# Optimization experiments

Hardware: AMD Instinct MI355X
Metric: run time of the kernel (lower is better)

Reference implementation:

```python
import jax, jax.numpy as jnp
import numpy as np

B, H, S, D = 2, 16, 1024, 64  # batch, n_heads, seq_len, d_k
NEG = -1.0e9


def setup_inputs() -> dict:
    key = jax.random.key(0)
    kq, kk, kv, kt, kf, km, kd = jax.random.split(key, 7)
    Q = jax.random.normal(kq, (B, H, S, D), dtype=jnp.float32)
    K = jax.random.normal(kk, (B, H, S, D), dtype=jnp.float32)
    V = jax.random.normal(kv, (B, H, S, D), dtype=jnp.float32)
    ia_type = jax.random.normal(kt, (B, H, S, S), dtype=jnp.float32)
    ia_feat = jax.random.normal(kf, (B, H, S, S), dtype=jnp.float32)
    attn_mask_if = jax.random.bernoulli(km, 0.1, (B, H, S, S))
    attn_mask = attn_mask_if  # passed to forward but unused, as in the source
    distance_matrix = jax.random.normal(kd, (B, S, S), dtype=jnp.float32)
    return {"Q": Q, "K": K, "V": V, "attn_mask": attn_mask,
            "attn_mask_if": attn_mask_if, "ia_type": ia_type,
            "ia_feat": ia_feat, "distance_matrix": distance_matrix}


def reference(Q, K, V, attn_mask, attn_mask_if, ia_type, ia_feat, distance_matrix):
    # scores1 = Q K^T / sqrt(d_k)
    scores1 = jnp.einsum("bhqd,bhkd->bhqk", Q, K) / jnp.sqrt(jnp.float32(D))
    # bias masked to -1e9, then scores masked again to -1e9 => masked entries are exactly -1e9
    scores = jnp.where(attn_mask_if, NEG, scores1 + ia_type + ia_feat)
    attn = jax.nn.softmax(scores, axis=-1)
    context = jnp.einsum("bhqk,bhkd->bhqd", attn, V)
    return context, attn
```

## Files before the change

### kernel.cpp

```cpp
#include <hip/hip_runtime.h>
#include <math.h>

#define S_LEN 1024
#define D_DIM 64
#define NEGV  (-1.0e9f)

__global__ __launch_bounds__(256, 2)
void attn_bias_fused(const float* __restrict__ Q, const float* __restrict__ K,
                     const float* __restrict__ V, const int* __restrict__ mif,
                     const float* __restrict__ iat, const float* __restrict__ iaf,
                     float* __restrict__ ctx, float* __restrict__ attn)
{
    __shared__ float4 Kt4[D_DIM][64];
    __shared__ float  SB[2048];

    float* Pn = (float*)Kt4;
    float (*Qst)[16] = (float(*)[16])SB;

    const int tid  = threadIdx.x;
    const int wave = tid >> 6;
    const int lane = tid & 63;
    const int bh   = blockIdx.x >> 6;
    const int qb   = (blockIdx.x & 63) << 4;

    const float* Qb = Q + ((size_t)(bh * S_LEN + qb)) * D_DIM;
    const float* Kb = K + ((size_t)bh * S_LEN) * D_DIM;
    const float* Vb = V + ((size_t)bh * S_LEN) * D_DIM;

    {
        int q = tid >> 4, l = tid & 15;
        float4 v = *(const float4*)(Qb + (size_t)q * D_DIM + l * 4);
        Qst[4 * l + 0][q] = v.x;
        Qst[4 * l + 1][q] = v.y;
        Qst[4 * l + 2][q] = v.z;
        Qst[4 * l + 3][q] = v.w;
    }

    const int kg = lane;
    const int qg = wave;

    float4 sc[16];

    #pragma unroll
    for (int c = 0; c < 4; ++c) {
        __syncthreads();
        {
            int l = tid & 15, kr0 = tid >> 4;
            #pragma unroll
            for (int i = 0; i < 16; ++i) {
                int kk = i * 16 + kr0;
                float4 v = *(const float4*)(Kb + (size_t)(c * 256 + kk) * D_DIM + l * 4);
                int cc  = (kk >> 2) ^ (l & 7);
                int sub = kk & 3;
                ((float*)&Kt4[4 * l + 0][cc])[sub] = v.x;
                ((float*)&Kt4[4 * l + 1][cc])[sub] = v.y;
                ((float*)&Kt4[4 * l + 2][cc])[sub] = v.z;
                ((float*)&Kt4[4 * l + 3][cc])[sub] = v.w;
            }
        }
        __syncthreads();

        float4 bt[4], bf[4];
        int4   bm[4];
        #pragma unroll
        for (int i = 0; i < 4; ++i) {
            size_t off = ((size_t)(bh * S_LEN + qb + qg * 4 + i)) * S_LEN + c * 256 + kg * 4;
            bt[i] = *(const float4*)(iat + off);
            bf[i] = *(const float4*)(iaf + off);
            bm[i] = *(const int4*)(mif + off);
        }

        float4 a0 = {0.f, 0.f, 0.f, 0.f}, a1 = a0, a2 = a0, a3 = a0;
        #pragma unroll 16
        for (int d = 0; d < D_DIM; ++d) {
            float4 kv = Kt4[d][kg ^ ((d >> 2) & 7)];
            float4 qv = *(const float4*)&Qst[d][qg * 4];
            a0.x = fmaf(qv.x, kv.x, a0.x); a0.y = fmaf(qv.x, kv.y, a0.y);
            a0.z = fmaf(qv.x, kv.z, a0.z); a0.w = fmaf(qv.x, kv.w, a0.w);
            a1.x = fmaf(qv.y, kv.x, a1.x); a1.y = fmaf(qv.y, kv.y, a1.y);
            a1.z = fmaf(qv.y, kv.z, a1.z); a1.w = fmaf(qv.y, kv.w, a1.w);
            a2.x = fmaf(qv.z, kv.x, a2.x); a2.y = fmaf(qv.z, kv.y, a2.y);
            a2.z = fmaf(qv.z, kv.z, a2.z); a2.w = fmaf(qv.z, kv.w, a2.w);
            a3.x = fmaf(qv.w, kv.x, a3.x); a3.y = fmaf(qv.w, kv.y, a3.y);
            a3.z = fmaf(qv.w, kv.z, a3.z); a3.w = fmaf(qv.w, kv.w, a3.w);
        }

        float4 av[4] = {a0, a1, a2, a3};
        #pragma unroll
        for (int i = 0; i < 4; ++i) {
            float4 s = av[i];
            float4 t = bt[i], f = bf[i];
            int4   m = bm[i];
            s.x = m.x ? NEGV : fmaf(s.x, 0.125f, t.x + f.x);
            s.y = m.y ? NEGV : fmaf(s.y, 0.125f, t.y + f.y);
            s.z = m.z ? NEGV : fmaf(s.z, 0.125f, t.z + f.z);
            s.w = m.w ? NEGV : fmaf(s.w, 0.125f, t.w + f.w);
            sc[c * 4 + i] = s;
        }
    }
    __syncthreads();

    {
        float mx[4], sum[4], rinv[4];
        #pragma unroll
        for (int i = 0; i < 4; ++i) {
            float m = -INFINITY;
            #pragma unroll
            for (int c = 0; c < 4; ++c) {
                float4 v = sc[c * 4 + i];
                m = fmaxf(m, fmaxf(fmaxf(v.x, v.y), fmaxf(v.z, v.w)));
            }
            #pragma unroll
            for (int s = 1; s < 64; s <<= 1) m = fmaxf(m, __shfl_xor(m, s, 64));
            mx[i] = m;
        }
        #pragma unroll
        for (int i = 0; i < 4; ++i) {
            float sm = 0.f;
            #pragma unroll
            for (int c = 0; c < 4; ++c) {
                float4 v = sc[c * 4 + i];
                v.x = __expf(v.x - mx[i]);
                v.y = __expf(v.y - mx[i]);
                v.z = __expf(v.z - mx[i]);
                v.w = __expf(v.w - mx[i]);
                sc[c * 4 + i] = v;
                sm += v.x + v.y + v.z + v.w;
            }
            #pragma unroll
            for (int s = 1; s < 64; s <<= 1) sm += __shfl_xor(sm, s, 64);
            sum[i] = sm;
            rinv[i] = 1.f / sm;
        }
        #pragma unroll
        for (int i = 0; i < 4; ++i) {
            int r = qg * 4 + i;
            float* arow = attn + ((size_t)(bh * S_LEN + qb + r)) * S_LEN;
            #pragma unroll
            for (int c = 0; c < 4; ++c) {
                float4 v = sc[c * 4 + i];
                v.x *= rinv[i]; v.y *= rinv[i]; v.z *= rinv[i]; v.w *= rinv[i];
                *(float4*)(arow + c * 256 + kg * 4)  = v;
                *(float4*)&Pn[r * 1024 + c * 256 + kg * 4] = v;
            }
        }
        (void)sum;
    }
    __syncthreads();

    {
        int dg = lane & 15;
        int ks = lane >> 4;
        float4 acc[16];
        #pragma unroll
        for (int q = 0; q < 16; ++q) acc[q] = make_float4(0.f, 0.f, 0.f, 0.f);

        #pragma unroll 2
        for (int i = 0; i < 16; ++i) {
            int k0 = wave * 256 + i * 16 + ks * 4;
            const float* vrow = Vb + (size_t)k0 * D_DIM + dg * 4;
            float4 v0 = *(const float4*)(vrow + 0 * D_DIM);
            float4 v1 = *(const float4*)(vrow + 1 * D_DIM);
            float4 v2 = *(const float4*)(vrow + 2 * D_DIM);
            float4 v3 = *(const float4*)(vrow + 3 * D_DIM);
            #pragma unroll
            for (int q = 0; q < 16; ++q) {
                float4 p = *(const float4*)&Pn[q * 1024 + k0];
                float4 a = acc[q];
                a.x = fmaf(p.x, v0.x, a.x); a.x = fmaf(p.y, v1.x, a.x);
                a.x = fmaf(p.z, v2.x, a.x); a.x = fmaf(p.w, v3.x, a.x);
                a.y = fmaf(p.x, v0.y, a.y); a.y = fmaf(p.y, v1.y, a.y);
                a.y = fmaf(p.z, v2.y, a.y); a.y = fmaf(p.w, v3.y, a.y);
                a.z = fmaf(p.x, v0.z, a.z); a.z = fmaf(p.y, v1.z, a.z);
                a.z = fmaf(p.z, v2.z, a.z); a.z = fmaf(p.w, v3.z, a.z);
                a.w = fmaf(p.x, v0.w, a.w); a.w = fmaf(p.y, v1.w, a.w);
                a.w = fmaf(p.z, v2.w, a.w); a.w = fmaf(p.w, v3.w, a.w);
                acc[q] = a;
            }
        }

        #pragma unroll
        for (int q = 0; q < 16; ++q) {
            acc[q].x += __shfl_xor(acc[q].x, 16, 64);
            acc[q].y += __shfl_xor(acc[q].y, 16, 64);
            acc[q].z += __shfl_xor(acc[q].z, 16, 64);
            acc[q].w += __shfl_xor(acc[q].w, 16, 64);
            acc[q].x += __shfl_xor(acc[q].x, 32, 64);
            acc[q].y += __shfl_xor(acc[q].y, 32, 64);
            acc[q].z += __shfl_xor(acc[q].z, 32, 64);
            acc[q].w += __shfl_xor(acc[q].w, 32, 64);
        }

        float* scratch = SB;
        #pragma unroll
        for (int qh = 0; qh < 2; ++qh) {
            __syncthreads();
            if (lane < 16) {
                #pragma unroll
                for (int j = 0; j < 8; ++j)
                    *(float4*)&scratch[(wave * 8 + j) * 64 + dg * 4] = acc[qh * 8 + j];
            }
            __syncthreads();
            if (tid < 128) {
                int qq = tid >> 4;
                int dr = tid & 15;
                float4 r = make_float4(0.f, 0.f, 0.f, 0.f);
                #pragma unroll
                for (int s = 0; s < 4; ++s) {
                    float4 v = *(const float4*)&scratch[(s * 8 + qq) * 64 + dr * 4];
                    r.x += v.x; r.y += v.y; r.z += v.z; r.w += v.w;
                }
                *(float4*)(ctx + ((size_t)(bh * S_LEN + qb + qh * 8 + qq)) * D_DIM + dr * 4) = r;
            }
        }
    }
}

extern "C" void kernel_launch(void* const* d_in, const int* in_sizes, int n_in,
                              void* d_out, int out_size, void* d_ws, size_t ws_size,
                              hipStream_t stream) {
    const float* Q   = (const float*)d_in[0];
    const float* K   = (const float*)d_in[1];
    const float* V   = (const float*)d_in[2];
    const int*   mif = (const int*)d_in[4];
    const float* iat = (const float*)d_in[5];
    const float* iaf = (const float*)d_in[6];

    float* ctx  = (float*)d_out;
    float* attn = (float*)d_out + (size_t)2 * 16 * 1024 * 64;

    dim3 grid(2048), block(256);
    hipLaunchKernelGGL(attn_bias_fused, grid, block, 0, stream,
                       Q, K, V, mif, iat, iaf, ctx, attn);
}
```

Baseline: 536.8 us.

## Use 512-thread blocks of 32 query rows and read P back from global

Each block now has 512 threads and covers 32 query rows instead of 16, so every K tile staged in shared memory serves twice as many rows. The normalized probabilities are no longer copied into LDS; the P·V stage reads them back from the attn output just written to global memory. The context reduction is restructured so all waves write partial sums to a larger scratch area before one final reduction, which removes several barriers. Risks: the much tighter launch bound (512, 4) likely caps VGPRs low enough to cause spills with 16 float4 score registers, and P now costs extra L2 traffic.

```diff
diff --git a/kernel.cpp b/kernel.cpp
--- a/kernel.cpp
+++ b/kernel.cpp
@@ -5,7 +5,7 @@
 #define D_DIM 64
 #define NEGV  (-1.0e9f)
 
-__global__ __launch_bounds__(256, 2)
+__global__ __launch_bounds__(512, 4)
 void attn_bias_fused(const float* __restrict__ Q, const float* __restrict__ K,
                      const float* __restrict__ V, const int* __restrict__ mif,
                      const float* __restrict__ iat, const float* __restrict__ iaf,
@@ -14,14 +14,14 @@
     __shared__ float4 Kt4[D_DIM][64];
     __shared__ float  SB[2048];
 
-    float* Pn = (float*)Kt4;
-    float (*Qst)[16] = (float(*)[16])SB;
+    float (*Qst)[32] = (float(*)[32])SB;
+    float* scr = (float*)Kt4;
 
     const int tid  = threadIdx.x;
     const int wave = tid >> 6;
     const int lane = tid & 63;
-    const int bh   = blockIdx.x >> 6;
-    const int qb   = (blockIdx.x & 63) << 4;
+    const int bh   = blockIdx.x >> 5;
+    const int qb   = (blockIdx.x & 31) << 5;
 
     const float* Qb = Q + ((size_t)(bh * S_LEN + qb)) * D_DIM;
     const float* Kb = K + ((size_t)bh * S_LEN) * D_DIM;
@@ -47,8 +47,8 @@
         {
             int l = tid & 15, kr0 = tid >> 4;
             #pragma unroll
-            for (int i = 0; i < 16; ++i) {
-                int kk = i * 16 + kr0;
+            for (int i = 0; i < 8; ++i) {
+                int kk = i * 32 + kr0;
                 float4 v = *(const float4*)(Kb + (size_t)(c * 256 + kk) * D_DIM + l * 4);
                 int cc  = (kk >> 2) ^ (l & 7);
                 int sub = kk & 3;
@@ -98,7 +98,6 @@
             sc[c * 4 + i] = s;
         }
     }
-    __syncthreads();
 
     {
         float mx[4], sum[4], rinv[4];
@@ -140,8 +139,7 @@
             for (int c = 0; c < 4; ++c) {
                 float4 v = sc[c * 4 + i];
                 v.x *= rinv[i]; v.y *= rinv[i]; v.z *= rinv[i]; v.w *= rinv[i];
-                *(float4*)(arow + c * 256 + kg * 4)  = v;
-                *(float4*)&Pn[r * 1024 + c * 256 + kg * 4] = v;
+                *(float4*)(arow + c * 256 + kg * 4) = v;
             }
         }
         (void)sum;
@@ -149,70 +147,71 @@
     __syncthreads();
 
     {
-        int dg = lane & 15;
-        int ks = lane >> 4;
-        float4 acc[16];
-        #pragma unroll
-        for (int q = 0; q < 16; ++q) acc[q] = make_float4(0.f, 0.f, 0.f, 0.f);
-
-        #pragma unroll 2
-        for (int i = 0; i < 16; ++i) {
-            int k0 = wave * 256 + i * 16 + ks * 4;
-            const float* vrow = Vb + (size_t)k0 * D_DIM + dg * 4;
-            float4 v0 = *(const float4*)(vrow + 0 * D_DIM);
-            float4 v1 = *(const float4*)(vrow + 1 * D_DIM);
-            float4 v2 = *(const float4*)(vrow + 2 * D_DIM);
-            float4 v3 = *(const float4*)(vrow + 3 * D_DIM);
+        const int dg = lane & 15;
+        const int ks = lane >> 4;
+        for (int h = 0; h < 2; ++h) {
+            float4 acc[16];
+            #pragma unroll
+            for (int q = 0; q < 16; ++q) acc[q] = make_float4(0.f, 0.f, 0.f, 0.f);
+
+            const float* pb = attn + ((size_t)(bh * S_LEN + qb + h * 16)) * S_LEN;
+
+            #pragma unroll 2
+            for (int i = 0; i < 8; ++i) {
+                int k0 = wave * 128 + i * 16 + ks * 4;
+                const float* vrow = Vb + (size_t)k0 * D_DIM + dg * 4;
+                float4 v0 = *(const float4*)(vrow + 0 * D_DIM);
+                float4 v1 = *(const float4*)(vrow + 1 * D_DIM);
+                float4 v2 = *(const float4*)(vrow + 2 * D_DIM);
+                float4 v3 = *(const float4*)(vrow + 3 * D_DIM);
+                #pragma unroll
+                for (int q = 0; q < 16; ++q) {
+                    float4 p = *(const float4*)(pb + (size_t)q * S_LEN + k0);
+                    float4 a = acc[q];
+                    a.x = fmaf(p.x, v0.x, a.x); a.x = fmaf(p.y, v1.x, a.x);
+                    a.x = fmaf(p.z, v2.x, a.x); a.x = fmaf(p.w, v3.x, a.x);
+                    a.y = fmaf(p.x, v0.y, a.y); a.y = fmaf(p.y, v1.y, a.y);
+                    a.y = fmaf(p.z, v2.y, a.y); a.y = fmaf(p.w, v3.y, a.y);
+                    a.z = fmaf(p.x, v0.z, a.z); a.z = fmaf(p.y, v1.z, a.z);
+                    a.z = fmaf(p.z, v2.z, a.z); a.z = fmaf(p.w, v3.z, a.z);
+                    a.w = fmaf(p.x, v0.w, a.w); a.w = fmaf(p.y, v1.w, a.w);
+                    a.w = fmaf(p.z, v2.w, a.w); a.w = fmaf(p.w, v3.w, a.w);
+                    acc[q] = a;
+                }
+            }
+
             #pragma unroll
             for (int q = 0; q < 16; ++q) {
-                float4 p = *(const float4*)&Pn[q * 1024 + k0];
-                float4 a = acc[q];
-                a.x = fmaf(p.x, v0.x, a.x); a.x = fmaf(p.y, v1.x, a.x);
-                a.x = fmaf(p.z, v2.x, a.x); a.x = fmaf(p.w, v3.x, a.x);
-                a.y = fmaf(p.x, v0.y, a.y); a.y = fmaf(p.y, v1.y, a.y);
-                a.y = fmaf(p.z, v2.y, a.y); a.y = fmaf(p.w, v3.y, a.y);
-                a.z = fmaf(p.x, v0.z, a.z); a.z = fmaf(p.y, v1.z, a.z);
-                a.z = fmaf(p.z, v2.z, a.z); a.z = fmaf(p.w, v3.z, a.z);
-                a.w = fmaf(p.x, v0.w, a.w); a.w = fmaf(p.y, v1.w, a.w);
-                a.w = fmaf(p.z, v2.w, a.w); a.w = fmaf(p.w, v3.w, a.w);
-                acc[q] = a;
-            }
-        }
-
-        #pragma unroll
-        for (int q = 0; q < 16; ++q) {
-            acc[q].x += __shfl_xor(acc[q].x, 16, 64);
-            acc[q].y += __shfl_xor(acc[q].y, 16, 64);
-            acc[q].z += __shfl_xor(acc[q].z, 16, 64);
-            acc[q].w += __shfl_xor(acc[q].w, 16, 64);
-            acc[q].x += __shfl_xor(acc[q].x, 32, 64);
-            acc[q].y += __shfl_xor(acc[q].y, 32, 64);
-            acc[q].z += __shfl_xor(acc[q].z, 32, 64);
-            acc[q].w += __shfl_xor(acc[q].w, 32, 64);
-        }
-
-        float* scratch = SB;
-        #pragma unroll
-        for (int qh = 0; qh < 2; ++qh) {
-            __syncthreads();
+                acc[q].x += __shfl_xor(acc[q].x, 16, 64);
+                acc[q].y += __shfl_xor(acc[q].y, 16, 64);
+                acc[q].z += __shfl_xor(acc[q].z, 16, 64);
+                acc[q].w += __shfl_xor(acc[q].w, 16, 64);
+                acc[q].x += __shfl_xor(acc[q].x, 32, 64);
+                acc[q].y += __shfl_xor(acc[q].y, 32, 64);
+                acc[q].z += __shfl_xor(acc[q].z, 32, 64);
+                acc[q].w += __shfl_xor(acc[q].w, 32, 64);
+            }
+
             if (lane < 16) {
                 #pragma unroll
-                for (int j = 0; j < 8; ++j)
-                    *(float4*)&scratch[(wave * 8 + j) * 64 + dg * 4] = acc[qh * 8 + j];
-            }
-            __syncthreads();
-            if (tid < 128) {
-                int qq = tid >> 4;
-                int dr = tid & 15;
-                float4 r = make_float4(0.f, 0.f, 0.f, 0.f);
-                #pragma unroll
-                for (int s = 0; s < 4; ++s) {
-                    float4 v = *(const float4*)&scratch[(s * 8 + qq) * 64 + dr * 4];
-                    r.x += v.x; r.y += v.y; r.z += v.z; r.w += v.w;
-                }
-                *(float4*)(ctx + ((size_t)(bh * S_LEN + qb + qh * 8 + qq)) * D_DIM + dr * 4) = r;
-            }
-        }
+                for (int q = 0; q < 16; ++q)
+                    *(float4*)&scr[((h * 8 + wave) * 16 + q) * 64 + dg * 4] = acc[q];
+            }
+        }
+    }
+    __syncthreads();
+
+    {
+        int qq = tid >> 4;
+        int dq = tid & 15;
+        int h  = qq >> 4, q = qq & 15;
+        float4 r = make_float4(0.f, 0.f, 0.f, 0.f);
+        #pragma unroll
+        for (int w = 0; w < 8; ++w) {
+            float4 v = *(const float4*)&scr[((h * 8 + w) * 16 + q) * 64 + dq * 4];
+            r.x += v.x; r.y += v.y; r.z += v.z; r.w += v.w;
+        }
+        *(float4*)(ctx + ((size_t)(bh * S_LEN + qb + qq)) * D_DIM + dq * 4) = r;
     }
 }
 
@@ -229,7 +228,7 @@
     float* ctx  = (float*)d_out;
     float* attn = (float*)d_out + (size_t)2 * 16 * 1024 * 64;
 
-    dim3 grid(2048), block(256);
+    dim3 grid(1024), block(512);
     hipLaunchKernelGGL(attn_bias_fused, grid, block, 0, stream,
                        Q, K, V, mif, iat, iaf, ctx, attn);
 }
```

Measured after the change: 719.6 us. +34.1%, slower.

## Halve shared memory, re-read P from global, raise occupancy and swizzle blocks

Applied to the files above, without the earlier changes.

Shared memory drops from 72KB to 36KB. K is staged in two 32-wide d halves, and the normalized probabilities are no longer kept in LDS; the PV phase reads them back from the just-written attn output in global memory. Launch bounds rise to 4 blocks per CU, and block indices are swizzled so neighbouring blocks work on different heads. Bias loads are split so the mask is loaded after the QK product to ease register pressure. Risks are extra global or L2 traffic for the P reads, register spills at the higher occupancy target, and reliance on a block reading its own global writes after a syncthreads.

```diff
diff --git a/kernel.cpp b/kernel.cpp
--- a/kernel.cpp
+++ b/kernel.cpp
@@ -5,23 +5,26 @@
 #define D_DIM 64
 #define NEGV  (-1.0e9f)
 
-__global__ __launch_bounds__(256, 2)
+__global__ __launch_bounds__(256, 4)
 void attn_bias_fused(const float* __restrict__ Q, const float* __restrict__ K,
                      const float* __restrict__ V, const int* __restrict__ mif,
                      const float* __restrict__ iat, const float* __restrict__ iaf,
                      float* __restrict__ ctx, float* __restrict__ attn)
 {
-    __shared__ float4 Kt4[D_DIM][64];
-    __shared__ float  SB[2048];
-
-    float* Pn = (float*)Kt4;
+    __shared__ float4 Kt4[32][64];
+    __shared__ float  SB[1024];
+
     float (*Qst)[16] = (float(*)[16])SB;
+    float* scr = (float*)Kt4;
 
     const int tid  = threadIdx.x;
     const int wave = tid >> 6;
     const int lane = tid & 63;
-    const int bh   = blockIdx.x >> 6;
-    const int qb   = (blockIdx.x & 63) << 4;
+
+    const int blk = blockIdx.x;
+    const int swz = ((blk & 7) << 8) | (blk >> 3);
+    const int bh  = swz >> 6;
+    const int qb  = (swz & 63) << 4;
 
     const float* Qb = Q + ((size_t)(bh * S_LEN + qb)) * D_DIM;
     const float* Kb = K + ((size_t)bh * S_LEN) * D_DIM;
@@ -43,46 +46,60 @@
 
     #pragma unroll
     for (int c = 0; c < 4; ++c) {
-        __syncthreads();
-        {
-            int l = tid & 15, kr0 = tid >> 4;
-            #pragma unroll
-            for (int i = 0; i < 16; ++i) {
-                int kk = i * 16 + kr0;
-                float4 v = *(const float4*)(Kb + (size_t)(c * 256 + kk) * D_DIM + l * 4);
-                int cc  = (kk >> 2) ^ (l & 7);
-                int sub = kk & 3;
-                ((float*)&Kt4[4 * l + 0][cc])[sub] = v.x;
-                ((float*)&Kt4[4 * l + 1][cc])[sub] = v.y;
-                ((float*)&Kt4[4 * l + 2][cc])[sub] = v.z;
-                ((float*)&Kt4[4 * l + 3][cc])[sub] = v.w;
-            }
-        }
-        __syncthreads();
-
         float4 bt[4], bf[4];
-        int4   bm[4];
-        #pragma unroll
-        for (int i = 0; i < 4; ++i) {
-            size_t off = ((size_t)(bh * S_LEN + qb + qg * 4 + i)) * S_LEN + c * 256 + kg * 4;
-            bt[i] = *(const float4*)(iat + off);
-            bf[i] = *(const float4*)(iaf + off);
+        float4 a0 = {0.f, 0.f, 0.f, 0.f}, a1 = a0, a2 = a0, a3 = a0;
+
+        #pragma unroll
+        for (int h = 0; h < 2; ++h) {
+            __syncthreads();
+            {
+                int l2 = tid & 7, kr0 = tid >> 3;
+                #pragma unroll
+                for (int i = 0; i < 8; ++i) {
+                    int kk = i * 32 + kr0;
+                    float4 v = *(const float4*)(Kb + (size_t)(c * 256 + kk) * D_DIM
+                                                + h * 32 + l2 * 4);
+                    int cc  = (kk >> 2) ^ l2;
+                    int sub = kk & 3;
+                    ((float*)&Kt4[4 * l2 + 0][cc])[sub] = v.x;
+                    ((float*)&Kt4[4 * l2 + 1][cc])[sub] = v.y;
+                    ((float*)&Kt4[4 * l2 + 2][cc])[sub] = v.z;
+                    ((float*)&Kt4[4 * l2 + 3][cc])[sub] = v.w;
+                }
+            }
+            __syncthreads();
+
+            if (h == 0) {
+                #pragma unroll
+                for (int i = 0; i < 4; ++i) {
+                    size_t off = ((size_t)(bh * S_LEN + qb + qg * 4 + i)) * S_LEN
+                               + c * 256 + kg * 4;
+                    bt[i] = *(const float4*)(iat + off);
+                    bf[i] = *(const float4*)(iaf + off);
+                }
+            }
+
+            #pragma unroll 16
+            for (int dd = 0; dd < 32; ++dd) {
+                float4 kv = Kt4[dd][kg ^ ((dd >> 2) & 7)];
+                float4 qv = *(const float4*)&Qst[h * 32 + dd][qg * 4];
+                a0.x = fmaf(qv.x, kv.x, a0.x); a0.y = fmaf(qv.x, kv.y, a0.y);
+                a0.z = fmaf(qv.x, kv.z, a0.z); a0.w = fmaf(qv.x, kv.w, a0.w);
+                a1.x = fmaf(qv.y, kv.x, a1.x); a1.y = fmaf(qv.y, kv.y, a1.y);
+                a1.z = fmaf(qv.y, kv.z, a1.z); a1.w = fmaf(qv.y, kv.w, a1.w);
+                a2.x = fmaf(qv.z, kv.x, a2.x); a2.y = fmaf(qv.z, kv.y, a2.y);
+                a2.z = fmaf(qv.z, kv.z, a2.z); a2.w = fmaf(qv.z, kv.w, a2.w);
+                a3.x = fmaf(qv.w, kv.x, a3.x); a3.y = fmaf(qv.w, kv.y, a3.y);
+                a3.z = fmaf(qv.w, kv.z, a3.z); a3.w = fmaf(qv.w, kv.w, a3.w);
+            }
+        }
+
+        int4 bm[4];
+        #pragma unroll
+        for (int i = 0; i < 4; ++i) {
+            size_t off = ((size_t)(bh * S_LEN + qb + qg * 4 + i)) * S_LEN
+                       + c * 256 + kg * 4;
             bm[i] = *(const int4*)(mif + off);
-        }
-
-        float4 a0 = {0.f, 0.f, 0.f, 0.f}, a1 = a0, a2 = a0, a3 = a0;
-        #pragma unroll 16
-        for (int d = 0; d < D_DIM; ++d) {
-            float4 kv = Kt4[d][kg ^ ((d >> 2) & 7)];
-            float4 qv = *(const float4*)&Qst[d][qg * 4];
-            a0.x = fmaf(qv.x, kv.x, a0.x); a0.y = fmaf(qv.x, kv.y, a0.y);
-            a0.z = fmaf(qv.x, kv.z, a0.z); a0.w = fmaf(qv.x, kv.w, a0.w);
-            a1.x = fmaf(qv.y, kv.x, a1.x); a1.y = fmaf(qv.y, kv.y, a1.y);
-            a1.z = fmaf(qv.y, kv.z, a1.z); a1.w = fmaf(qv.y, kv.w, a1.w);
-            a2.x = fmaf(qv.z, kv.x, a2.x); a2.y = fmaf(qv.z, kv.y, a2.y);
-            a2.z = fmaf(qv.z, kv.z, a2.z); a2.w = fmaf(qv.z, kv.w, a2.w);
-            a3.x = fmaf(qv.w, kv.x, a3.x); a3.y = fmaf(qv.w, kv.y, a3.y);
-            a3.z = fmaf(qv.w, kv.z, a3.z); a3.w = fmaf(qv.w, kv.w, a3.w);
         }
 
         float4 av[4] = {a0, a1, a2, a3};
@@ -98,10 +115,9 @@
             sc[c * 4 + i] = s;
         }
     }
-    __syncthreads();
 
     {
-        float mx[4], sum[4], rinv[4];
+        float mx[4], rinv[4];
         #pragma unroll
         for (int i = 0; i < 4; ++i) {
             float m = -INFINITY;
@@ -129,7 +145,6 @@
             }
             #pragma unroll
             for (int s = 1; s < 64; s <<= 1) sm += __shfl_xor(sm, s, 64);
-            sum[i] = sm;
             rinv[i] = 1.f / sm;
         }
         #pragma unroll
@@ -140,20 +155,20 @@
             for (int c = 0; c < 4; ++c) {
                 float4 v = sc[c * 4 + i];
                 v.x *= rinv[i]; v.y *= rinv[i]; v.z *= rinv[i]; v.w *= rinv[i];
-                *(float4*)(arow + c * 256 + kg * 4)  = v;
-                *(float4*)&Pn[r * 1024 + c * 256 + kg * 4] = v;
-            }
-        }
-        (void)sum;
+                *(float4*)(arow + c * 256 + kg * 4) = v;
+            }
+        }
     }
     __syncthreads();
 
     {
-        int dg = lane & 15;
-        int ks = lane >> 4;
+        const int dg = lane & 15;
+        const int ks = lane >> 4;
         float4 acc[16];
         #pragma unroll
         for (int q = 0; q < 16; ++q) acc[q] = make_float4(0.f, 0.f, 0.f, 0.f);
+
+        const float* pb = attn + ((size_t)(bh * S_LEN + qb)) * S_LEN;
 
         #pragma unroll 2
         for (int i = 0; i < 16; ++i) {
@@ -165,7 +180,7 @@
             float4 v3 = *(const float4*)(vrow + 3 * D_DIM);
             #pragma unroll
             for (int q = 0; q < 16; ++q) {
-                float4 p = *(const float4*)&Pn[q * 1024 + k0];
+                float4 p = *(const float4*)(pb + (size_t)q * S_LEN + k0);
                 float4 a = acc[q];
                 a.x = fmaf(p.x, v0.x, a.x); a.x = fmaf(p.y, v1.x, a.x);
                 a.x = fmaf(p.z, v2.x, a.x); a.x = fmaf(p.w, v3.x, a.x);
@@ -191,14 +206,13 @@
             acc[q].w += __shfl_xor(acc[q].w, 32, 64);
         }
 
-        float* scratch = SB;
         #pragma unroll
         for (int qh = 0; qh < 2; ++qh) {
             __syncthreads();
             if (lane < 16) {
                 #pragma unroll
                 for (int j = 0; j < 8; ++j)
-                    *(float4*)&scratch[(wave * 8 + j) * 64 + dg * 4] = acc[qh * 8 + j];
+                    *(float4*)&scr[(wave * 8 + j) * 64 + dg * 4] = acc[qh * 8 + j];
             }
             __syncthreads();
             if (tid < 128) {
@@ -207,7 +221,7 @@
                 float4 r = make_float4(0.f, 0.f, 0.f, 0.f);
                 #pragma unroll
                 for (int s = 0; s < 4; ++s) {
-                    float4 v = *(const float4*)&scratch[(s * 8 + qq) * 64 + dr * 4];
+                    float4 v = *(const float4*)&scr[(s * 8 + qq) * 64 + dr * 4];
                     r.x += v.x; r.y += v.y; r.z += v.z; r.w += v.w;
                 }
                 *(float4*)(ctx + ((size_t)(bh * S_LEN + qb + qh * 8 + qq)) * D_DIM + dr * 4) = r;
```

Measured after the change: 937.3 us. 1.75x slower.
